# Performance work log

Measured on AMD Instinct MI355X. Metric: run time of the kernel, lower is better.

## Reference

```python
import jax, jax.numpy as jnp
import numpy as np

N = 8192
C = 256


def setup_inputs() -> dict:
    key = jax.random.key(0)
    k_x, k_wr, k_br, k_wc, k_bc = jax.random.split(key, 5)
    scale = 1.0 / np.sqrt(C)
    return {
        "x": jax.random.normal(k_x, (N, C), dtype=jnp.float32),
        "w_reduce": jax.random.uniform(k_wr, (C, C), dtype=jnp.float32, minval=-scale, maxval=scale),
        "b_reduce": jax.random.uniform(k_br, (C,), dtype=jnp.float32, minval=-scale, maxval=scale),
        "w_contr": jax.random.uniform(k_wc, (1, C), dtype=jnp.float32, minval=-scale, maxval=scale),
        "b_contr": jax.random.uniform(k_bc, (1,), dtype=jnp.float32, minval=-scale, maxval=scale),
    }


def reference(x, w_reduce, b_reduce, w_contr, b_contr):
    # Original math: y_ij = reduce(x_i + x_j); z_ij = sigmoid(contr(y_ij));
    # out_i = mean_j y_ij * z_ij.
    # Since reduce/contr are affine, decompose without the [N,N,C] tensor:
    #   y_ij = r_i + r_j + b_reduce,        r = x @ Wr^T
    #   contr(y_ij) = s_i + s_j + c0,       s = r . wc, c0 = b_reduce . wc + bc
    n = x.shape[0]
    r = x @ w_reduce.T                                   # [N, C]
    wc = w_contr[0]                                      # [C]
    s = r @ wc                                           # [N]
    c0 = b_reduce @ wc + b_contr[0]                      # scalar
    Z = jax.nn.sigmoid(s[:, None] + s[None, :] + c0)     # [N, N] pairwise gate
    m = jnp.mean(Z, axis=1, keepdims=True)               # [N, 1]
    # mean_j (r_i + r_j + b) * z_ij = (r_i + b) * m_i + (Z @ r)_i / N
    out = (r + b_reduce) * m + (Z @ r) / n               # [N, C]
    return out
```

## Files before the change

kernel.cpp:

```cpp
#include <hip/hip_runtime.h>
#include <hip/hip_bf16.h>
#include <stdint.h>

#define NN 8192
#define CC 256
#define NSPLIT 8
#define JR (NN / NSPLIT)
#define NITER (JR / 32)

typedef float f32x4 __attribute__((ext_vector_type(4)));
typedef float f32x2 __attribute__((ext_vector_type(2)));
typedef short s16x8 __attribute__((ext_vector_type(8)));

#define LOG2E 1.4426950408889634f

#define OFF_WT  0
#define OFF_R   (OFF_WT + CC*CC)
#define OFF_S2  (OFF_R + NN*CC)
#define OFF_C0  (OFF_S2 + NN)
#define OFF_SS  (OFF_C0 + 16)
#define OFF_V   (OFF_SS + NSPLIT*NN)
#define OFF_RB  (OFF_V + (NSPLIT*NN*CC)/2)

__global__ __launch_bounds__(256) void k_prep(const float* __restrict__ w,
                                              const float* __restrict__ br,
                                              const float* __restrict__ wcv,
                                              const float* __restrict__ bc,
                                              float* __restrict__ ws) {
  int k = blockIdx.x, c = threadIdx.x;
  ws[OFF_WT + k * CC + c] = w[c * CC + k];
  if (blockIdx.x == 0 && threadIdx.x < 64) {
    int lane = threadIdx.x;
    f32x4 b4 = *(const f32x4*)&br[lane * 4];
    f32x4 w4 = *(const f32x4*)&wcv[lane * 4];
    float d = b4[0]*w4[0] + b4[1]*w4[1] + b4[2]*w4[2] + b4[3]*w4[3];
    #pragma unroll
    for (int m = 32; m >= 1; m >>= 1) d += __shfl_xor(d, m, 64);
    if (lane == 0) { ws[OFF_C0] = d + bc[0]; ws[OFF_C0 + 1] = (d + bc[0]) * LOG2E; }
  }
}

__global__ __launch_bounds__(256) void k_r(const float* __restrict__ x,
                                           float* __restrict__ ws) {
  __shared__ float xs[64][260];
  int bi = blockIdx.x;
  int rowblk = bi >> 2, colblk = bi & 3;
  int tid = threadIdx.x;
  int i0 = rowblk * 64;
  for (int t = tid; t < 64 * 64; t += 256) {
    int rr = t >> 6, c4 = t & 63;
    *(f32x4*)&xs[rr][c4 * 4] = *(const f32x4*)&x[(i0 + rr) * CC + c4 * 4];
  }
  __syncthreads();
  int tx = tid & 15, ty = tid >> 4;
  int cbase = colblk * 64 + tx * 4;
  int r0 = ty * 4;
  float acc[4][4] = {};
  const float* wt = ws + OFF_WT;
  for (int k = 0; k < CC; k += 2) {
    f32x4 wv0 = *(const f32x4*)&wt[k * CC + cbase];
    f32x4 wv1 = *(const f32x4*)&wt[(k + 1) * CC + cbase];
    f32x2 xv[4];
    #pragma unroll
    for (int rr = 0; rr < 4; rr++) xv[rr] = *(const f32x2*)&xs[r0 + rr][k];
    #pragma unroll
    for (int rr = 0; rr < 4; rr++)
      #pragma unroll
      for (int cc = 0; cc < 4; cc++)
        acc[rr][cc] = fmaf(xv[rr][1], wv1[cc], fmaf(xv[rr][0], wv0[cc], acc[rr][cc]));
  }
  unsigned short* rb = (unsigned short*)(ws + OFF_RB);
  #pragma unroll
  for (int rr = 0; rr < 4; rr++) {
    int j = i0 + r0 + rr;
    f32x4 o = {acc[rr][0], acc[rr][1], acc[rr][2], acc[rr][3]};
    *(f32x4*)&ws[OFF_R + j * CC + cbase] = o;
    #pragma unroll
    for (int cc = 0; cc < 4; cc++) {
      int c = cbase + cc;
      unsigned u = __float_as_uint(acc[rr][cc]);
      u = (u + 0x7fffu + ((u >> 16) & 1u)) >> 16;
      int idx = (((j >> 5) * 16 + (c >> 4)) * 64 + ((j >> 3) & 3) * 16 + (c & 15)) * 8 + (j & 7);
      rb[idx] = (unsigned short)u;
    }
  }
}

__global__ __launch_bounds__(256) void k_s(const float* __restrict__ wcv,
                                           float* __restrict__ ws) {
  int tid = threadIdx.x;
  int lane = tid & 63;
  int row = blockIdx.x * 4 + (tid >> 6);
  f32x4 rv = *(const f32x4*)&ws[OFF_R + row * CC + lane * 4];
  f32x4 wv = *(const f32x4*)&wcv[lane * 4];
  float d = rv[0]*wv[0] + rv[1]*wv[1] + rv[2]*wv[2] + rv[3]*wv[3];
  #pragma unroll
  for (int m = 32; m >= 1; m >>= 1) d += __shfl_xor(d, m, 64);
  if (lane == 0) ws[OFF_S2 + row] = d * LOG2E;
}


#define STAGE(BUF, IT) { \
  const char* gb_ = rbase + (size_t)(IT) * 16384 + w * 1024 + l * 16; \
  _Pragma("unroll") \
  for (int q_ = 0; q_ < 4; q_++) \
    __builtin_amdgcn_global_load_lds( \
      (const __attribute__((address_space(1))) void*)(gb_ + q_ * 4096), \
      (__attribute__((address_space(3))) void*)&ldsb[(BUF) * 16384 + w * 1024 + q_ * 4096], \
      16, 0, 0); }

#define WAITBAR4 { asm volatile("s_waitcnt vmcnt(4)" ::: "memory"); \
  __builtin_amdgcn_s_barrier(); \
  __builtin_amdgcn_sched_barrier(0); }

#define WAITBAR0 { asm volatile("s_waitcnt vmcnt(0)" ::: "memory"); \
  __builtin_amdgcn_s_barrier(); \
  __builtin_amdgcn_sched_barrier(0); }

#define SIGMOID(IT, AFA, AFB) { \
  f32x4 sj0_ = *(const f32x4*)&s2l[(IT) * 32 + g * 8]; \
  f32x4 sj1_ = *(const f32x4*)&s2l[(IT) * 32 + g * 8 + 4]; \
  _Pragma("unroll") \
  for (int t_ = 0; t_ < 8; t_++) { \
    float sj_ = (t_ < 4) ? sj0_[t_] : sj1_[t_ - 4]; \
    float eA_, eB_; \
    asm("v_exp_f32 %0, %1" : "=v"(eA_) : "v"(negaA - sj_)); \
    asm("v_exp_f32 %0, %1" : "=v"(eB_) : "v"(negaB - sj_)); \
    float zA_ = __builtin_amdgcn_rcpf(1.0f + eA_); \
    float zB_ = __builtin_amdgcn_rcpf(1.0f + eB_); \
    unsigned uA_ = __float_as_uint(zA_); \
    uA_ = (uA_ + 0x7fffu + ((uA_ >> 16) & 1u)) >> 16; \
    (AFA)[t_] = (short)uA_; \
    unsigned uB_ = __float_as_uint(zB_); \
    uB_ = (uB_ + 0x7fffu + ((uB_ >> 16) & 1u)) >> 16; \
    (AFB)[t_] = (short)uB_; } }

#define MFMA_PHASE(AFA, AFB, LP) { \
  __builtin_amdgcn_s_setprio(1); \
  _Pragma("unroll") \
  for (int ct_ = 0; ct_ < 16; ct_++) { \
    s16x8 bf_ = *(const s16x8*)((LP) + ct_ * 1024 + l * 16); \
    accA[ct_] = __builtin_amdgcn_mfma_f32_16x16x32_bf16(AFA, bf_, accA[ct_], 0, 0, 0); \
    accB[ct_] = __builtin_amdgcn_mfma_f32_16x16x32_bf16(AFB, bf_, accB[ct_], 0, 0, 0); } \
  acc1A = __builtin_amdgcn_mfma_f32_16x16x32_bf16(AFA, ones, acc1A, 0, 0, 0); \
  acc1B = __builtin_amdgcn_mfma_f32_16x16x32_bf16(AFB, ones, acc1B, 0, 0, 0); \
  __builtin_amdgcn_s_setprio(0); }

__global__ __launch_bounds__(256, 2) void k_main(float* __restrict__ ws) {
  __shared__ char ldsb[3 * 16384];
  __shared__ float s2l[1024];
  int blk = blockIdx.x;
  int rt = blk >> 3, h = blk & 7;
  int tid = threadIdx.x;
  int w = tid >> 6, l = tid & 63;
  int lr = l & 15, g = l >> 4;
  int iw = rt * 128 + w * 32;
  float c02 = ws[OFF_C0 + 1];
  float negaA = -(ws[OFF_S2 + iw + lr] + c02);
  float negaB = -(ws[OFF_S2 + iw + 16 + lr] + c02);

  const float* s2p = ws + OFF_S2 + h * JR;
  *(f32x4*)&s2l[tid * 4] = *(const f32x4*)(s2p + tid * 4);
  __syncthreads();

  f32x4 accA[16], accB[16], acc1A, acc1B;
  #pragma unroll
  for (int i = 0; i < 16; i++) { accA[i] = (f32x4)(0.f); accB[i] = (f32x4)(0.f); }
  acc1A = (f32x4)(0.f); acc1B = (f32x4)(0.f);
  s16x8 ones;
  #pragma unroll
  for (int t = 0; t < 8; t++) ones[t] = (short)0x3F80;

  const char* rbase = (const char*)(ws + OFF_RB) + (size_t)h * (JR * CC * 2);

  STAGE(0, 0);
  STAGE(1, 1);
  s16x8 afA0, afB0, afA1, afB1;
  SIGMOID(0, afA0, afB0);

  for (int it = 0; it < NITER - 2; it += 2) {
    const char* lp0 = ldsb + (it % 3) * 16384;
    SIGMOID(it + 1, afA1, afB1);
    WAITBAR4;
    STAGE((it + 2) % 3, it + 2);
    MFMA_PHASE(afA0, afB0, lp0);
    const char* lp1 = ldsb + ((it + 1) % 3) * 16384;
    SIGMOID(it + 2, afA0, afB0);
    WAITBAR4;
    STAGE((it + 3) % 3, it + 3);
    MFMA_PHASE(afA1, afB1, lp1);
  }
  {
    const char* lp = ldsb + ((NITER - 2) % 3) * 16384;
    SIGMOID(NITER - 1, afA1, afB1);
    WAITBAR4;
    MFMA_PHASE(afA0, afB0, lp);
  }
  {
    const char* lp = ldsb + ((NITER - 1) % 3) * 16384;
    WAITBAR0;
    MFMA_PHASE(afA1, afB1, lp);
  }

  if (lr == 0) {
    #pragma unroll
    for (int q = 0; q < 4; q++) {
      ws[OFF_SS + h * NN + iw + g * 4 + q] = acc1A[q];
      ws[OFF_SS + h * NN + iw + 16 + g * 4 + q] = acc1B[q];
    }
  }
  unsigned short* Vb = (unsigned short*)(ws + OFF_V);
  size_t vbase = (size_t)h * (NN * CC);
  #pragma unroll
  for (int ct = 0; ct < 16; ct++) {
    #pragma unroll
    for (int q = 0; q < 4; q++) {
      unsigned uA = __float_as_uint(accA[ct][q]);
      uA = (uA + 0x7fffu + ((uA >> 16) & 1u)) >> 16;
      Vb[vbase + (size_t)(iw + g * 4 + q) * CC + ct * 16 + lr] = (unsigned short)uA;
      unsigned uB = __float_as_uint(accB[ct][q]);
      uB = (uB + 0x7fffu + ((uB >> 16) & 1u)) >> 16;
      Vb[vbase + (size_t)(iw + 16 + g * 4 + q) * CC + ct * 16 + lr] = (unsigned short)uB;
    }
  }
}

__global__ __launch_bounds__(256) void k_epi(const float* __restrict__ br,
                                             const float* __restrict__ ws,
                                             float* __restrict__ out) {
  int idx = blockIdx.x * 256 + threadIdx.x;
  int i = idx >> 5, c8 = (idx & 31) * 8;
  float S = 0.f;
  #pragma unroll
  for (int p = 0; p < NSPLIT; p++) S += ws[OFF_SS + p * NN + i];
  float m = S * (1.0f / NN);
  float v[8] = {};
  const unsigned short* Vb = (const unsigned short*)(ws + OFF_V);
  #pragma unroll
  for (int p = 0; p < NSPLIT; p++) {
    s16x8 pv = *(const s16x8*)&Vb[(size_t)p * (NN * CC) + (size_t)i * CC + c8];
    #pragma unroll
    for (int t = 0; t < 8; t++)
      v[t] += __uint_as_float(((unsigned)(unsigned short)pv[t]) << 16);
  }
  f32x4 r0 = *(const f32x4*)&ws[OFF_R + (size_t)i * CC + c8];
  f32x4 r1 = *(const f32x4*)&ws[OFF_R + (size_t)i * CC + c8 + 4];
  f32x4 b0 = *(const f32x4*)&br[c8];
  f32x4 b1 = *(const f32x4*)&br[c8 + 4];
  f32x4 o0, o1;
  #pragma unroll
  for (int t = 0; t < 4; t++) {
    o0[t] = (r0[t] + b0[t]) * m + v[t] * (1.0f / NN);
    o1[t] = (r1[t] + b1[t]) * m + v[t + 4] * (1.0f / NN);
  }
  *(f32x4*)&out[(size_t)i * CC + c8] = o0;
  *(f32x4*)&out[(size_t)i * CC + c8 + 4] = o1;
}

extern "C" void kernel_launch(void* const* d_in, const int* in_sizes, int n_in,
                              void* d_out, int out_size, void* d_ws, size_t ws_size,
                              hipStream_t stream) {
  const float* x  = (const float*)d_in[0];
  const float* w  = (const float*)d_in[1];
  const float* br = (const float*)d_in[2];
  const float* wc = (const float*)d_in[3];
  const float* bc = (const float*)d_in[4];
  float* ws = (float*)d_ws;
  float* out = (float*)d_out;
  (void)in_sizes; (void)n_in; (void)out_size; (void)ws_size;

  k_prep<<<256, 256, 0, stream>>>(w, br, wc, bc, ws);
  k_r<<<512, 256, 0, stream>>>(x, ws);
  k_s<<<2048, 256, 0, stream>>>(wc, ws);
  k_main<<<512, 256, 0, stream>>>(ws);
  k_epi<<<1024, 256, 0, stream>>>(br, ws, out);
}
```

Measured before the change: 93.77 us.

## Enlarge main tile to 64 rows per wave, fuse s into r kernel

```diff
diff --git a/kernel.cpp b/kernel.cpp
--- a/kernel.cpp
+++ b/kernel.cpp
@@ -6,7 +6,8 @@
 #define CC 256
 #define NSPLIT 8
 #define JR (NN / NSPLIT)
-#define NITER (JR / 32)
+#define CH 64
+#define NITER (JR / CH)
 
 typedef float f32x4 __attribute__((ext_vector_type(4)));
 typedef float f32x2 __attribute__((ext_vector_type(2)));
@@ -16,8 +17,8 @@
 
 #define OFF_WT  0
 #define OFF_R   (OFF_WT + CC*CC)
-#define OFF_S2  (OFF_R + NN*CC)
-#define OFF_C0  (OFF_S2 + NN)
+#define OFF_S   (OFF_R + NN*CC)
+#define OFF_C0  (OFF_S + NN)
 #define OFF_SS  (OFF_C0 + 16)
 #define OFF_V   (OFF_SS + NSPLIT*NN)
 #define OFF_RB  (OFF_V + (NSPLIT*NN*CC)/2)
@@ -27,21 +28,36 @@
                                               const float* __restrict__ wcv,
                                               const float* __restrict__ bc,
                                               float* __restrict__ ws) {
-  int k = blockIdx.x, c = threadIdx.x;
-  ws[OFF_WT + k * CC + c] = w[c * CC + k];
-  if (blockIdx.x == 0 && threadIdx.x < 64) {
+  __shared__ float t[32][33];
+  int bi = blockIdx.x;
+  int tr = bi >> 3, tc = bi & 7;
+  int tx = threadIdx.x & 31, ty = threadIdx.x >> 5;
+  #pragma unroll
+  for (int p = 0; p < 4; p++) {
+    int row = ty + p * 8;
+    t[row][tx] = w[(tr * 32 + row) * CC + tc * 32 + tx];
+  }
+  __syncthreads();
+  #pragma unroll
+  for (int p = 0; p < 4; p++) {
+    int row = ty + p * 8;
+    ws[OFF_WT + (tc * 32 + row) * CC + tr * 32 + tx] = t[tx][row];
+  }
+  if (bi < 32) ws[OFF_S + bi * 256 + threadIdx.x] = 0.f;
+  if (bi == 0 && threadIdx.x < 64) {
     int lane = threadIdx.x;
     f32x4 b4 = *(const f32x4*)&br[lane * 4];
     f32x4 w4 = *(const f32x4*)&wcv[lane * 4];
     float d = b4[0]*w4[0] + b4[1]*w4[1] + b4[2]*w4[2] + b4[3]*w4[3];
     #pragma unroll
     for (int m = 32; m >= 1; m >>= 1) d += __shfl_xor(d, m, 64);
-    if (lane == 0) { ws[OFF_C0] = d + bc[0]; ws[OFF_C0 + 1] = (d + bc[0]) * LOG2E; }
-  }
-}
-
-__global__ __launch_bounds__(256) void k_r(const float* __restrict__ x,
-                                           float* __restrict__ ws) {
+    if (lane == 0) ws[OFF_C0] = d + bc[0];
+  }
+}
+
+__global__ __launch_bounds__(256) void k_rs(const float* __restrict__ x,
+                                            const float* __restrict__ wcv,
+                                            float* __restrict__ ws) {
   __shared__ float xs[64][260];
   int bi = blockIdx.x;
   int rowblk = bi >> 2, colblk = bi & 3;
@@ -70,6 +86,7 @@
         acc[rr][cc] = fmaf(xv[rr][1], wv1[cc], fmaf(xv[rr][0], wv0[cc], acc[rr][cc]));
   }
   unsigned short* rb = (unsigned short*)(ws + OFF_RB);
+  f32x4 wc4 = *(const f32x4*)&wcv[cbase];
   #pragma unroll
   for (int rr = 0; rr < 4; rr++) {
     int j = i0 + r0 + rr;
@@ -83,33 +100,24 @@
       int idx = (((j >> 5) * 16 + (c >> 4)) * 64 + ((j >> 3) & 3) * 16 + (c & 15)) * 8 + (j & 7);
       rb[idx] = (unsigned short)u;
     }
-  }
-}
-
-__global__ __launch_bounds__(256) void k_s(const float* __restrict__ wcv,
-                                           float* __restrict__ ws) {
-  int tid = threadIdx.x;
-  int lane = tid & 63;
-  int row = blockIdx.x * 4 + (tid >> 6);
-  f32x4 rv = *(const f32x4*)&ws[OFF_R + row * CC + lane * 4];
-  f32x4 wv = *(const f32x4*)&wcv[lane * 4];
-  float d = rv[0]*wv[0] + rv[1]*wv[1] + rv[2]*wv[2] + rv[3]*wv[3];
-  #pragma unroll
-  for (int m = 32; m >= 1; m >>= 1) d += __shfl_xor(d, m, 64);
-  if (lane == 0) ws[OFF_S2 + row] = d * LOG2E;
-}
-
-
-#define STAGE(BUF, IT) { \
-  const char* gb_ = rbase + (size_t)(IT) * 16384 + w * 1024 + l * 16; \
+    float sd = acc[rr][0]*wc4[0] + acc[rr][1]*wc4[1] + acc[rr][2]*wc4[2] + acc[rr][3]*wc4[3];
+    atomicAdd(&ws[OFF_S + j], sd);
+  }
+}
+
+
+union U8 { s16x8 v; unsigned u[4]; };
+
+#define STAGE(SLOT, IT) { \
+  const char* gb_ = rbase + (size_t)(IT) * 32768 + w * 8192 + l * 16; \
   _Pragma("unroll") \
-  for (int q_ = 0; q_ < 4; q_++) \
+  for (int q_ = 0; q_ < 8; q_++) \
     __builtin_amdgcn_global_load_lds( \
-      (const __attribute__((address_space(1))) void*)(gb_ + q_ * 4096), \
-      (__attribute__((address_space(3))) void*)&ldsb[(BUF) * 16384 + w * 1024 + q_ * 4096], \
+      (const __attribute__((address_space(1))) void*)(gb_ + q_ * 1024), \
+      (__attribute__((address_space(3))) void*)&ldsb[(SLOT) * 32768 + w * 8192 + q_ * 1024 + l * 16], \
       16, 0, 0); }
 
-#define WAITBAR4 { asm volatile("s_waitcnt vmcnt(4)" ::: "memory"); \
+#define WAITBAR8 { asm volatile("s_waitcnt vmcnt(8)" ::: "memory"); \
   __builtin_amdgcn_s_barrier(); \
   __builtin_amdgcn_sched_barrier(0); }
 
@@ -117,112 +125,135 @@
   __builtin_amdgcn_s_barrier(); \
   __builtin_amdgcn_sched_barrier(0); }
 
-#define SIGMOID(IT, AFA, AFB) { \
-  f32x4 sj0_ = *(const f32x4*)&s2l[(IT) * 32 + g * 8]; \
-  f32x4 sj1_ = *(const f32x4*)&s2l[(IT) * 32 + g * 8 + 4]; \
+#define SB0 __builtin_amdgcn_sched_barrier(0);
+
+#define SIG(ITC, AF) { \
+  int itc_ = (ITC); \
   _Pragma("unroll") \
-  for (int t_ = 0; t_ < 8; t_++) { \
-    float sj_ = (t_ < 4) ? sj0_[t_] : sj1_[t_ - 4]; \
-    float eA_, eB_; \
-    asm("v_exp_f32 %0, %1" : "=v"(eA_) : "v"(negaA - sj_)); \
-    asm("v_exp_f32 %0, %1" : "=v"(eB_) : "v"(negaB - sj_)); \
-    float zA_ = __builtin_amdgcn_rcpf(1.0f + eA_); \
-    float zB_ = __builtin_amdgcn_rcpf(1.0f + eB_); \
-    unsigned uA_ = __float_as_uint(zA_); \
-    uA_ = (uA_ + 0x7fffu + ((uA_ >> 16) & 1u)) >> 16; \
-    (AFA)[t_] = (short)uA_; \
-    unsigned uB_ = __float_as_uint(zB_); \
-    uB_ = (uB_ + 0x7fffu + ((uB_ >> 16) & 1u)) >> 16; \
-    (AFB)[t_] = (short)uB_; } }
-
-#define MFMA_PHASE(AFA, AFB, LP) { \
-  __builtin_amdgcn_s_setprio(1); \
+  for (int kh_ = 0; kh_ < 2; kh_++) { \
+    f32x4 a0_ = *(const f32x4*)&s2l[itc_ * CH + kh_ * 32 + g * 8]; \
+    f32x4 a1_ = *(const f32x4*)&s2l[itc_ * CH + kh_ * 32 + g * 8 + 4]; \
+    _Pragma("unroll") \
+    for (int f_ = 0; f_ < 4; f_++) { \
+      float z_[8]; \
+      _Pragma("unroll") \
+      for (int t_ = 0; t_ < 8; t_++) { \
+        float sj_ = (t_ < 4) ? a0_[t_] : a1_[t_ - 4]; \
+        float e_; \
+        asm("v_exp_f32 %0, %1" : "=v"(e_) : "v"(nega[f_] - sj_)); \
+        float zz_ = __builtin_amdgcn_rcpf(1.0f + e_); \
+        ssum[f_] += zz_; \
+        z_[t_] = zz_; \
+      } \
+      U8 u8_; \
+      asm("v_cvt_pk_bf16_f32 %0, %1, %2" : "=v"(u8_.u[0]) : "v"(z_[0]), "v"(z_[1])); \
+      asm("v_cvt_pk_bf16_f32 %0, %1, %2" : "=v"(u8_.u[1]) : "v"(z_[2]), "v"(z_[3])); \
+      asm("v_cvt_pk_bf16_f32 %0, %1, %2" : "=v"(u8_.u[2]) : "v"(z_[4]), "v"(z_[5])); \
+      asm("v_cvt_pk_bf16_f32 %0, %1, %2" : "=v"(u8_.u[3]) : "v"(z_[6]), "v"(z_[7])); \
+      AF[f_][kh_] = u8_.v; \
+    } \
+  } }
+
+#define MF(AF, SLOT) { \
+  const char* lp_ = ldsb + (SLOT) * 32768; \
   _Pragma("unroll") \
-  for (int ct_ = 0; ct_ < 16; ct_++) { \
-    s16x8 bf_ = *(const s16x8*)((LP) + ct_ * 1024 + l * 16); \
-    accA[ct_] = __builtin_amdgcn_mfma_f32_16x16x32_bf16(AFA, bf_, accA[ct_], 0, 0, 0); \
-    accB[ct_] = __builtin_amdgcn_mfma_f32_16x16x32_bf16(AFB, bf_, accB[ct_], 0, 0, 0); } \
-  acc1A = __builtin_amdgcn_mfma_f32_16x16x32_bf16(AFA, ones, acc1A, 0, 0, 0); \
-  acc1B = __builtin_amdgcn_mfma_f32_16x16x32_bf16(AFB, ones, acc1B, 0, 0, 0); \
-  __builtin_amdgcn_s_setprio(0); }
-
-__global__ __launch_bounds__(256, 2) void k_main(float* __restrict__ ws) {
-  __shared__ char ldsb[3 * 16384];
-  __shared__ float s2l[1024];
+  for (int kh_ = 0; kh_ < 2; kh_++) \
+    _Pragma("unroll") \
+    for (int ct_ = 0; ct_ < 16; ct_++) { \
+      s16x8 bf_ = *(const s16x8*)(lp_ + kh_ * 16384 + ct_ * 1024 + l * 16); \
+      _Pragma("unroll") \
+      for (int f_ = 0; f_ < 4; f_++) \
+        acc[f_][ct_] = __builtin_amdgcn_mfma_f32_16x16x32_bf16(AF[f_][kh_], bf_, acc[f_][ct_], 0, 0, 0); \
+    } }
+
+__global__ __launch_bounds__(256, 1) void k_main(float* __restrict__ ws) {
+  __shared__ char ldsb[3 * 32768];
+  __shared__ float s2l[JR];
   int blk = blockIdx.x;
   int rt = blk >> 3, h = blk & 7;
   int tid = threadIdx.x;
   int w = tid >> 6, l = tid & 63;
   int lr = l & 15, g = l >> 4;
-  int iw = rt * 128 + w * 32;
-  float c02 = ws[OFF_C0 + 1];
-  float negaA = -(ws[OFF_S2 + iw + lr] + c02);
-  float negaB = -(ws[OFF_S2 + iw + 16 + lr] + c02);
-
-  const float* s2p = ws + OFF_S2 + h * JR;
-  *(f32x4*)&s2l[tid * 4] = *(const f32x4*)(s2p + tid * 4);
+  int iw = rt * 256 + w * 64;
+  float c0v = ws[OFF_C0];
+
+  const float* sp = ws + OFF_S + h * JR;
+  {
+    f32x4 sv = *(const f32x4*)(sp + tid * 4);
+    f32x4 so = {sv[0] * LOG2E, sv[1] * LOG2E, sv[2] * LOG2E, sv[3] * LOG2E};
+    *(f32x4*)&s2l[tid * 4] = so;
+  }
+  float nega[4];
+  #pragma unroll
+  for (int f = 0; f < 4; f++)
+    nega[f] = -(ws[OFF_S + iw + f * 16 + lr] + c0v) * LOG2E;
   __syncthreads();
 
-  f32x4 accA[16], accB[16], acc1A, acc1B;
-  #pragma unroll
-  for (int i = 0; i < 16; i++) { accA[i] = (f32x4)(0.f); accB[i] = (f32x4)(0.f); }
-  acc1A = (f32x4)(0.f); acc1B = (f32x4)(0.f);
-  s16x8 ones;
-  #pragma unroll
-  for (int t = 0; t < 8; t++) ones[t] = (short)0x3F80;
+  f32x4 acc[4][16];
+  #pragma unroll
+  for (int f = 0; f < 4; f++)
+    #pragma unroll
+    for (int ct = 0; ct < 16; ct++) acc[f][ct] = (f32x4)(0.f);
+  float ssum[4] = {0.f, 0.f, 0.f, 0.f};
 
   const char* rbase = (const char*)(ws + OFF_RB) + (size_t)h * (JR * CC * 2);
 
   STAGE(0, 0);
   STAGE(1, 1);
-  s16x8 afA0, afB0, afA1, afB1;
-  SIGMOID(0, afA0, afB0);
-
-  for (int it = 0; it < NITER - 2; it += 2) {
-    const char* lp0 = ldsb + (it % 3) * 16384;
-    SIGMOID(it + 1, afA1, afB1);
-    WAITBAR4;
-    STAGE((it + 2) % 3, it + 2);
-    MFMA_PHASE(afA0, afB0, lp0);
-    const char* lp1 = ldsb + ((it + 1) % 3) * 16384;
-    SIGMOID(it + 2, afA0, afB0);
-    WAITBAR4;
-    STAGE((it + 3) % 3, it + 3);
-    MFMA_PHASE(afA1, afB1, lp1);
+  s16x8 afA[4][2], afB[4][2];
+  SIG(0, afA);
+
+  int sA = 0;
+  #pragma unroll 1
+  for (int J = 0; J < NITER - 2; J += 2) {
+    int sB = sA + 1; if (sB == 3) sB = 0;
+    int sC = sB + 1; if (sC == 3) sC = 0;
+
+    WAITBAR8;
+    STAGE(sC, J + 2);
+    SB0;
+    SIG(J + 1, afB);
+    MF(afA, sA);
+
+    WAITBAR8;
+    STAGE(sA, J + 3);
+    SB0;
+    SIG(J + 2, afA);
+    MF(afB, sB);
+
+    sA = sC;
   }
   {
-    const char* lp = ldsb + ((NITER - 2) % 3) * 16384;
-    SIGMOID(NITER - 1, afA1, afB1);
-    WAITBAR4;
-    MFMA_PHASE(afA0, afB0, lp);
-  }
-  {
-    const char* lp = ldsb + ((NITER - 1) % 3) * 16384;
+    int sB = sA + 1; if (sB == 3) sB = 0;
+    WAITBAR8;
+    SIG(NITER - 1, afB);
+    MF(afA, sA);
     WAITBAR0;
-    MFMA_PHASE(afA1, afB1, lp);
-  }
-
-  if (lr == 0) {
-    #pragma unroll
-    for (int q = 0; q < 4; q++) {
-      ws[OFF_SS + h * NN + iw + g * 4 + q] = acc1A[q];
-      ws[OFF_SS + h * NN + iw + 16 + g * 4 + q] = acc1B[q];
-    }
+    MF(afB, sB);
+  }
+
+  #pragma unroll
+  for (int f = 0; f < 4; f++) {
+    ssum[f] += __shfl_xor(ssum[f], 16, 64);
+    ssum[f] += __shfl_xor(ssum[f], 32, 64);
+  }
+  if (l < 16) {
+    #pragma unroll
+    for (int f = 0; f < 4; f++)
+      ws[OFF_SS + h * NN + iw + f * 16 + lr] = ssum[f];
   }
   unsigned short* Vb = (unsigned short*)(ws + OFF_V);
   size_t vbase = (size_t)h * (NN * CC);
   #pragma unroll
-  for (int ct = 0; ct < 16; ct++) {
-    #pragma unroll
-    for (int q = 0; q < 4; q++) {
-      unsigned uA = __float_as_uint(accA[ct][q]);
-      uA = (uA + 0x7fffu + ((uA >> 16) & 1u)) >> 16;
-      Vb[vbase + (size_t)(iw + g * 4 + q) * CC + ct * 16 + lr] = (unsigned short)uA;
-      unsigned uB = __float_as_uint(accB[ct][q]);
-      uB = (uB + 0x7fffu + ((uB >> 16) & 1u)) >> 16;
-      Vb[vbase + (size_t)(iw + 16 + g * 4 + q) * CC + ct * 16 + lr] = (unsigned short)uB;
-    }
-  }
+  for (int f = 0; f < 4; f++)
+    #pragma unroll
+    for (int ct = 0; ct < 16; ct++)
+      #pragma unroll
+      for (int q = 0; q < 4; q++) {
+        unsigned u = __float_as_uint(acc[f][ct][q]);
+        u = (u + 0x7fffu + ((u >> 16) & 1u)) >> 16;
+        Vb[vbase + (size_t)(iw + f * 16 + g * 4 + q) * CC + ct * 16 + lr] = (unsigned short)u;
+      }
 }
 
 __global__ __launch_bounds__(256) void k_epi(const float* __restrict__ br,
@@ -269,9 +300,8 @@
   float* out = (float*)d_out;
   (void)in_sizes; (void)n_in; (void)out_size; (void)ws_size;
 
-  k_prep<<<256, 256, 0, stream>>>(w, br, wc, bc, ws);
-  k_r<<<512, 256, 0, stream>>>(x, ws);
-  k_s<<<2048, 256, 0, stream>>>(wc, ws);
-  k_main<<<512, 256, 0, stream>>>(ws);
+  k_prep<<<64, 256, 0, stream>>>(w, br, wc, bc, ws);
+  k_rs<<<512, 256, 0, stream>>>(x, wc, ws);
+  k_main<<<256, 256, 0, stream>>>(ws);
   k_epi<<<1024, 256, 0, stream>>>(br, ws, out);
 }
```

Measured after the change: 138.6 us. 47.8% more time.
